# Kernel optimization log

Measured on AMD Instinct MI355X. Metric: run time of the kernel, lower is better.

## Reference

```python
import jax, jax.numpy as jnp
import numpy as np

B, N, D, R = 2, 256, 128, 32

def _sh_l1(r):
    # e3nn-style component-normalized l=1 spherical harmonics of unit vectors
    return jnp.sqrt(3.0) * r

def _sh_l2(r):
    x, y, z = r[..., 0], r[..., 1], r[..., 2]
    c = jnp.sqrt(15.0)
    return jnp.stack([
        c * x * y,
        c * y * z,
        0.5 * jnp.sqrt(5.0) * (3.0 * z * z - 1.0),  # x^2+y^2+z^2 = 1
        c * x * z,
        0.5 * c * (x * x - y * y),
    ], axis=-1)

def _radial(rbf, w1, b1, w2, b2):
    h = rbf @ w1 + b1
    return (h * jax.nn.sigmoid(h)) @ w2 + b2  # Linear -> SiLU -> Linear

def _layernorm(x, g, b, eps=1e-5):
    m = jnp.mean(x, axis=-1, keepdims=True)
    v = jnp.var(x, axis=-1, keepdims=True)
    return (x - m) * jax.lax.rsqrt(v + eps) * g + b

def setup_inputs() -> dict:
    key = jax.random.key(0)
    ks = iter(jax.random.split(key, 40))
    def nrm(shape, s=1.0):
        return jax.random.normal(next(ks), shape, dtype=jnp.float32) * s
    r_hat = nrm((B, N, N, 3))
    r_hat = r_hat / (jnp.linalg.norm(r_hat, axis=-1, keepdims=True) + 1e-9)
    inp = {
        'node_s': nrm((B, N, D)),
        'node_v': nrm((B, N, 3, D)),
        'node_t': nrm((B, N, 5, D)),
        'rbf': jax.random.uniform(next(ks), (B, N, N, R), dtype=jnp.float32),
        'r_hat': r_hat,
        'mask': jnp.ones((B, N, N), dtype=jnp.float32),
    }
    s1, s2 = 1.0 / np.sqrt(R), 1.0 / np.sqrt(D)
    for p in ('r0', 'r1', 'r2', 'r110'):
        inp[p + '_w1'] = nrm((R, D), s1)
        inp[p + '_b1'] = jnp.zeros((D,), jnp.float32)
        inp[p + '_w2'] = nrm((D, D), s2)
        inp[p + '_b2'] = jnp.zeros((D,), jnp.float32)
    inp['src_w'] = nrm((D, D), s2)
    inp['ln_g'] = jnp.ones((D,), jnp.float32)
    inp['ln_b'] = jnp.zeros((D,), jnp.float32)
    inp['out_w'] = nrm((D, D), s2)
    inp['out_b'] = jnp.zeros((D,), jnp.float32)
    inp['v_scale'] = jnp.ones((D,), jnp.float32)
    inp['t_scale'] = jnp.ones((D,), jnp.float32)
    return inp

def reference(node_s, node_v, node_t, rbf, r_hat, mask,
              r0_w1, r0_b1, r0_w2, r0_b2,
              r1_w1, r1_b1, r1_w2, r1_b2,
              r2_w1, r2_b1, r2_w2, r2_b2,
              r110_w1, r110_b1, r110_w2, r110_b2,
              src_w, ln_g, ln_b, out_w, out_b, v_scale, t_scale):
    h = node_s @ src_w                               # (B,N,D)
    h_j = h[:, None, :, :] * mask[..., None]         # (B,N,N,D): h_j[b,i,j]=h[b,j]*mask[b,i,j]
    Y1 = _sh_l1(r_hat)                               # (B,N,N,3)
    Y2 = _sh_l2(r_hat)                               # (B,N,N,5)

    msg_s = jnp.sum(h_j * _radial(rbf, r0_w1, r0_b1, r0_w2, r0_b2), axis=2)  # (B,N,D)
    delta_v = jnp.einsum('bijd,bijc->bicd',
                         h_j * _radial(rbf, r1_w1, r1_b1, r1_w2, r1_b2), Y1) * v_scale
    delta_t = jnp.einsum('bijd,bijc->bicd',
                         h_j * _radial(rbf, r2_w1, r2_b1, r2_w2, r2_b2), Y2) * t_scale

    # v_j[b,i,j] = node_v[b,i] (per the torch unsqueeze(2).expand)
    dot_vY1 = jnp.einsum('bicd,bijc->bijd', node_v, Y1)                      # (B,N,N,D)
    msg_s_from_v = jnp.sum(dot_vY1 * _radial(rbf, r110_w1, r110_b1, r110_w2, r110_b2)
                           * mask[..., None], axis=2)                        # (B,N,D)

    delta_s = _layernorm(msg_s + msg_s_from_v, ln_g, ln_b) @ out_w + out_b
    return (delta_s, delta_v, delta_t)
```

## Files before the change

### kernel.cpp

```cpp
#include <hip/hip_runtime.h>

#define Bb 2
#define Nn 256
#define Dd 128
#define Rr 32

typedef unsigned short u16;
typedef unsigned int   u32;
typedef __attribute__((ext_vector_type(8))) short bf16x8;
typedef __attribute__((ext_vector_type(4))) float f32x4;
typedef __attribute__((ext_vector_type(2))) u32   u32x2;
typedef __attribute__((ext_vector_type(4))) u32   u32x4;

__device__ u16 g_w1t[4*Dd*Rr];
__device__ u16 g_w2t[4*Dd*Dd];

__device__ __forceinline__ short f2bfs(float f){
  u32 u = __float_as_uint(f);
  u += 0x7FFFu + ((u >> 16) & 1u);
  return (short)(u >> 16);
}
__device__ __forceinline__ u16 f2bf(float f){
  u32 u = __float_as_uint(f);
  u += 0x7FFFu + ((u >> 16) & 1u);
  return (u16)(u >> 16);
}
__device__ __forceinline__ u32 cvtpk(float a, float b){
  u32 r;
  asm("v_cvt_pk_bf16_f32 %0, %1, %2" : "=v"(r) : "v"(a), "v"(b));
  return r;
}
__device__ __forceinline__ int swz(int j){
  return (j&3) | ((((j>>2)^(j>>3))&1)<<2);
}

__global__ __launch_bounds__(128) void prep_kernel(
    const float* __restrict__ node_s, const float* __restrict__ src_w,
    const float* __restrict__ r0w1, const float* __restrict__ r1w1,
    const float* __restrict__ r2w1, const float* __restrict__ r3w1,
    const float* __restrict__ r0w2, const float* __restrict__ r1w2,
    const float* __restrict__ r2w2, const float* __restrict__ r3w2,
    float* __restrict__ h_out)
{
  const int bx = blockIdx.x;
  const int t  = threadIdx.x;
  if (bx < Bb*Nn){
    __shared__ float s_row[Dd];
    s_row[t] = node_s[(size_t)bx*Dd + t];
    __syncthreads();
    float acc = 0.f;
    #pragma unroll 8
    for (int k=0;k<Dd;k++) acc += s_row[k]*src_w[k*Dd + t];
    const int b = bx >> 8, i = bx & 255;
    h_out[(size_t)(b*Dd + t)*Nn + i] = acc;
  } else {
    const int kb = bx - Bb*Nn;
    const int p  = kb >> 3, sl = kb & 7;
    const float* W1 = (p==0)?r0w1:(p==1)?r1w1:(p==2)?r2w1:r3w1;
    const float* W2 = (p==0)?r0w2:(p==1)?r1w2:(p==2)?r2w2:r3w2;
    u16* W1T = g_w1t + p*Dd*Rr;
    u16* W2T = g_w2t + p*Dd*Dd;
    #pragma unroll
    for (int it=0; it<4; it++){
      int in = sl*512 + it*128 + t;
      W1T[(in & 127)*Rr + (in >> 7)] = f2bf(W1[in]);
    }
    #pragma unroll
    for (int it=0; it<16; it++){
      int in = sl*2048 + it*128 + t;
      W2T[(in & 127)*Dd + (in >> 7)] = f2bf(W2[in]);
    }
  }
}

__global__ __launch_bounds__(512,4) void se3_mfma13(
    const float* __restrict__ node_v,
    const float* __restrict__ rbf,
    const float* __restrict__ r_hat,
    const float* __restrict__ maskp,
    const float* __restrict__ r0b1, const float* __restrict__ r0b2,
    const float* __restrict__ r1b1, const float* __restrict__ r1b2,
    const float* __restrict__ r2b1, const float* __restrict__ r2b2,
    const float* __restrict__ r3b1, const float* __restrict__ r3b2,
    const float* __restrict__ ln_g, const float* __restrict__ ln_b,
    const float* __restrict__ out_w, const float* __restrict__ out_b,
    const float* __restrict__ v_scale, const float* __restrict__ t_scale,
    const float* __restrict__ h_ws,
    float* __restrict__ out_s, float* __restrict__ out_v, float* __restrict__ out_t)
{
  __shared__ u16   s_rbf[Nn*40];
  __shared__ u16   s_hid[2*64*128];
  __shared__ u16   s_YT[10*264];
  __shared__ u16   s_Y1r[3*264];
  __shared__ float s_msg[Dd];
  __shared__ float s_xn[Dd];
  __shared__ float s_part[4*Dd];
  __shared__ float s_mv[2];

  const int tid  = threadIdx.x;
  const int bi   = blockIdx.x;
  const int b    = bi >> 8;
  const int lane = tid & 63;
  const int w    = tid >> 6;
  const int q    = lane >> 4;
  const int cc   = lane & 15;
  const int dwb  = w*16;

  if (tid < Nn){
    int j = tid;
    size_t pidx = (size_t)bi*Nn + j;
    float mk = maskp[pidx];
    float x = r_hat[pidx*3+0];
    float y = r_hat[pidx*3+1];
    float z = r_hat[pidx*3+2];
    const float SQ3=1.7320508075688772f;
    const float C15=3.8729833462074170f;
    const float C5H=1.1180339887498949f;
    float y1a=SQ3*x, y1b=SQ3*y, y1c=SQ3*z;
    s_YT[0*264+j]=f2bf(mk);
    s_YT[1*264+j]=f2bf(y1a*mk);
    s_YT[2*264+j]=f2bf(y1b*mk);
    s_YT[3*264+j]=f2bf(y1c*mk);
    s_YT[4*264+j]=f2bf(C15*x*y*mk);
    s_YT[5*264+j]=f2bf(C15*y*z*mk);
    s_YT[6*264+j]=f2bf(C5H*(3.f*z*z-1.f)*mk);
    s_YT[7*264+j]=f2bf(C15*x*z*mk);
    s_YT[8*264+j]=f2bf(0.5f*C15*(x*x-y*y)*mk);
    s_YT[9*264+j]=f2bf(mk);
    s_Y1r[0*264+j]=f2bf(y1a);
    s_Y1r[1*264+j]=f2bf(y1b);
    s_Y1r[2*264+j]=f2bf(y1c);
  }

  const float* rbf_blk = rbf + (size_t)bi*Nn*Rr;
  const float* htb     = h_ws + (size_t)b*Dd*Nn;

  for (int idx=tid; idx<Nn*Rr/2; idx+=512){
    int j = idx >> 4, r2 = (idx & 15)*2;
    const float* src = &rbf_blk[j*Rr + r2];
    float v0 = src[0], v1 = src[1];
    *(u32*)&s_rbf[j*40 + r2] = cvtpk(v0, v1);
  }

  bf16x8 vBf;
  {
    const float* nv = node_v + (size_t)bi*3*Dd;
    int dd = dwb+cc;
    bf16x8 t = {0,0,0,0,0,0,0,0};
    if (q==0){
      t[0]=f2bfs(nv[0*Dd+dd]);
      t[1]=f2bfs(nv[1*Dd+dd]);
      t[2]=f2bfs(nv[2*Dd+dd]);
    }
    vBf=t;
  }

  __syncthreads();

  const f32x4 zf = {0.f,0.f,0.f,0.f};
  f32x4 accred = zf;
  const u16* ytrow = &s_YT[(cc<10?cc:9)*264];

  auto do_gemm1 = [&](int chn, int bufn, const bf16x8& w1f_, const f32x4& b1v_){
    #pragma unroll 1
    for (int jt=0;jt<4;jt++){
      const int jrow = jt*16 + cc;
      bf16x8 rbff = *(const bf16x8*)&s_rbf[(chn*64 + jrow)*40 + q*8];
      f32x4 hc = __builtin_amdgcn_mfma_f32_16x16x32_bf16(w1f_, rbff, zf, 0,0,0);
      float s[4];
      #pragma unroll
      for (int r=0;r<4;r++){
        float x  = hc[r] + b1v_[r];
        float e  = __expf(-x);
        s[r]     = x*__builtin_amdgcn_rcpf(1.f+e);
      }
      u32x2 pk = { cvtpk(s[0], s[1]), cvtpk(s[2], s[3]) };
      const int c0 = w*2 + (q>>1);
      *(u32x2*)&s_hid[bufn*8192 + jrow*128 + ((c0 ^ swz(jrow))<<3) + (q&1)*4] = pk;
    }
  };

  int buf = 0;
  bf16x8 w1f;  f32x4 b1v4;
  bf16x8 w2f[4]; float b2v; u32 gmask;

  w1f  = *(const bf16x8*)&g_w1t[(dwb+cc)*Rr + q*8];
  b1v4 = *(const f32x4*)&r0b1[dwb + q*4];
  do_gemm1(0, 0, w1f, b1v4);

  #pragma unroll 1
  for (int t=0;t<16;t++){
    const int p = t>>2, ch = t&3;
    if (ch==0){
      const u16* W2T = g_w2t + p*Dd*Dd;
      #pragma unroll
      for (int ks=0;ks<4;ks++)
        w2f[ks] = *(const bf16x8*)&W2T[(dwb+cc)*Dd + ks*32 + q*8];
      const float* B2p = (p==0)?r0b2:(p==1)?r1b2:(p==2)?r2b2:r3b2;
      b2v = B2p[dwb + cc];
      const int lo = (p==0)?0:(p==1)?1:(p==2)?4:9;
      const int hi = (p==0)?0:(p==1)?3:(p==2)?8:9;
      gmask = (cc>=lo && cc<=hi) ? 0xFFFFFFFFu : 0u;
    }
    __syncthreads();

    if (t<15){
      const int tn=t+1, pn=tn>>2, chn=tn&3;
      if (chn==0){
        w1f  = *(const bf16x8*)&g_w1t[pn*Dd*Rr + (dwb+cc)*Rr + q*8];
        const float* B1p = (pn==1)?r1b1:(pn==2)?r2b1:r3b1;
        b1v4 = *(const f32x4*)&B1p[dwb + q*4];
      }
      do_gemm1(chn, buf^1, w1f, b1v4);
    }

    #pragma unroll 1
    for (int g=0; g<2; g++){
      u32 bB[4];
      #pragma unroll 1
      for (int mm=0;mm<2;mm++){
        const int jp = g*32 + ((cc>>2)<<3) + mm*4 + (cc&3);
        bf16x8 af[4];
        #pragma unroll
        for (int ks=0;ks<4;ks++)
          af[ks] = *(const bf16x8*)&s_hid[buf*8192 + jp*128 + (((ks*4+q) ^ swz(jp))<<3)];

        f32x4 dotC;
        if (p==3){
          bf16x8 aY = {0,0,0,0,0,0,0,0};
          if (q==0){
            int jg = ch*64 + jp;
            aY[0]=(short)s_Y1r[0*264+jg];
            aY[1]=(short)s_Y1r[1*264+jg];
            aY[2]=(short)s_Y1r[2*264+jg];
          }
          dotC = __builtin_amdgcn_mfma_f32_16x16x32_bf16(aY, vBf, zf, 0,0,0);
        }

        f32x4 c2 = zf;
        #pragma unroll
        for (int ks=0;ks<4;ks++)
          c2 = __builtin_amdgcn_mfma_f32_16x16x32_bf16(af[ks], w2f[ks], c2, 0,0,0);
        float gg[4];
        if (p<3){
          f32x4 hq = *(const f32x4*)&htb[(size_t)(dwb+cc)*Nn + ch*64 + g*32 + q*8 + mm*4];
          #pragma unroll
          for (int r=0;r<4;r++)
            gg[r] = (c2[r]+b2v) * hq[r];
        } else {
          #pragma unroll
          for (int r=0;r<4;r++)
            gg[r] = (c2[r]+b2v) * dotC[r];
        }
        bB[mm*2+0] = cvtpk(gg[0], gg[1]);
        bB[mm*2+1] = cvtpk(gg[2], gg[3]);
      }
      bf16x8 aR = *(const bf16x8*)(ytrow + ch*64 + g*32 + q*8);
      u32* arp = (u32*)&aR;
      arp[0]&=gmask; arp[1]&=gmask; arp[2]&=gmask; arp[3]&=gmask;
      u32x4 bw = { bB[0], bB[1], bB[2], bB[3] };
      bf16x8 bG = __builtin_bit_cast(bf16x8, bw);
      accred = __builtin_amdgcn_mfma_f32_16x16x32_bf16(aR, bG, accred, 0,0,0);
    }
    buf ^= 1;
  }

  {
    const int d = dwb + cc;
    #pragma unroll
    for (int r=0;r<4;r++){
      const int rw = q*4 + r;
      float val = accred[r];
      if (rw==0)      s_msg[d] = val;
      else if (rw<=3) out_v[(size_t)bi*3*Dd + (size_t)(rw-1)*Dd + d] = val*v_scale[d];
      else if (rw<=8) out_t[(size_t)bi*5*Dd + (size_t)(rw-4)*Dd + d] = val*t_scale[d];
      else if (rw==9) s_xn[d] = val;
    }
  }
  __syncthreads();

  if (tid < 64){
    float a0=s_msg[tid]+s_xn[tid], a1=s_msg[tid+64]+s_xn[tid+64];
    float s1=a0+a1, s2=a0*a0+a1*a1;
    #pragma unroll
    for (int off=1;off<64;off<<=1){
      s1 += __shfl_xor(s1,off);
      s2 += __shfl_xor(s2,off);
    }
    if (tid==0){
      float m   = s1*(1.f/Dd);
      float var = fmaxf(s2*(1.f/Dd) - m*m, 0.f);
      s_mv[0]=m;
      s_mv[1]=rsqrtf(var+1e-5f);
    }
  }
  __syncthreads();
  if (tid < Dd){
    float msg = s_msg[tid]+s_xn[tid];
    s_xn[tid] = (msg - s_mv[0])*s_mv[1]*ln_g[tid] + ln_b[tid];
  }
  __syncthreads();

  {
    int dp = tid & 127, seg = tid >> 7;
    float pa = 0.f;
    #pragma unroll 8
    for (int k=seg*32;k<seg*32+32;k++)
      pa += s_xn[k]*out_w[k*Dd+dp];
    s_part[seg*Dd+dp]=pa;
  }
  __syncthreads();
  if (tid < Dd)
    out_s[(size_t)bi*Dd+tid] = s_part[tid]+s_part[Dd+tid]+s_part[2*Dd+tid]+s_part[3*Dd+tid]+out_b[tid];
}

extern "C" void kernel_launch(void* const* d_in, const int* in_sizes, int n_in,
                              void* d_out, int out_size, void* d_ws, size_t ws_size,
                              hipStream_t stream) {
  const float* node_s = (const float*)d_in[0];
  const float* node_v = (const float*)d_in[1];
  const float* rbf    = (const float*)d_in[3];
  const float* r_hat  = (const float*)d_in[4];
  const float* maskp  = (const float*)d_in[5];
  const float* r0w1=(const float*)d_in[6],  *r0b1=(const float*)d_in[7];
  const float* r0w2=(const float*)d_in[8],  *r0b2=(const float*)d_in[9];
  const float* r1w1=(const float*)d_in[10], *r1b1=(const float*)d_in[11];
  const float* r1w2=(const float*)d_in[12], *r1b2=(const float*)d_in[13];
  const float* r2w1=(const float*)d_in[14], *r2b1=(const float*)d_in[15];
  const float* r2w2=(const float*)d_in[16], *r2b2=(const float*)d_in[17];
  const float* r3w1=(const float*)d_in[18], *r3b1=(const float*)d_in[19];
  const float* r3w2=(const float*)d_in[20], *r3b2=(const float*)d_in[21];
  const float* src_w  =(const float*)d_in[22];
  const float* ln_g   =(const float*)d_in[23];
  const float* ln_b   =(const float*)d_in[24];
  const float* out_w  =(const float*)d_in[25];
  const float* out_b  =(const float*)d_in[26];
  const float* v_scale=(const float*)d_in[27];
  const float* t_scale=(const float*)d_in[28];

  float* h_ws = (float*)d_ws;
  float* out_s = (float*)d_out;
  float* out_v = out_s + (size_t)Bb*Nn*Dd;
  float* out_t = out_v + (size_t)Bb*Nn*3*Dd;

  prep_kernel<<<dim3(Bb*Nn + 32), dim3(128), 0, stream>>>(
      node_s, src_w,
      r0w1, r1w1, r2w1, r3w1, r0w2, r1w2, r2w2, r3w2,
      h_ws);
  se3_mfma13<<<dim3(Bb*Nn), dim3(512), 0, stream>>>(
      node_v, rbf, r_hat, maskp,
      r0b1,r0b2, r1b1,r1b2, r2b1,r2b2, r3b1,r3b2,
      ln_g, ln_b, out_w, out_b, v_scale, t_scale,
      h_ws, out_s, out_v, out_t);
}
```

Before: 184.5 us.

## Unroll chunk pipeline per radial net and pad hidden buffer instead of swizzle

Restructures the 16-step loop into an outer loop over the four radial nets with the four chunks manually unrolled, so each gemm1/gemm2 stage has constant buffer and chunk indices and the inner loops can be fully unrolled. The XOR swizzle on the shared hidden buffer is replaced by a padded row stride of 130, and the gather mask AND is replaced by pointing inactive lanes at an added zero row of Y. Per-chunk h loads are hoisted ahead of the MFMAs. The aim is less index arithmetic and more instruction-level overlap, at the cost of more registers and code size, which may hurt occupancy under the 512x4 launch bound.

```diff
diff --git a/kernel.cpp b/kernel.cpp
--- a/kernel.cpp
+++ b/kernel.cpp
@@ -29,9 +29,6 @@
   u32 r;
   asm("v_cvt_pk_bf16_f32 %0, %1, %2" : "=v"(r) : "v"(a), "v"(b));
   return r;
-}
-__device__ __forceinline__ int swz(int j){
-  return (j&3) | ((((j>>2)^(j>>3))&1)<<2);
 }
 
 __global__ __launch_bounds__(128) void prep_kernel(
@@ -73,7 +70,7 @@
   }
 }
 
-__global__ __launch_bounds__(512,4) void se3_mfma13(
+__global__ __launch_bounds__(512,4) void se3_mfma14(
     const float* __restrict__ node_v,
     const float* __restrict__ rbf,
     const float* __restrict__ r_hat,
@@ -89,8 +86,8 @@
     float* __restrict__ out_s, float* __restrict__ out_v, float* __restrict__ out_t)
 {
   __shared__ u16   s_rbf[Nn*40];
-  __shared__ u16   s_hid[2*64*128];
-  __shared__ u16   s_YT[10*264];
+  __shared__ u16   s_hid[2*64*130];
+  __shared__ u16   s_YT[11*264];
   __shared__ u16   s_Y1r[3*264];
   __shared__ float s_msg[Dd];
   __shared__ float s_xn[Dd];
@@ -104,6 +101,7 @@
   const int w    = tid >> 6;
   const int q    = lane >> 4;
   const int cc   = lane & 15;
+  const int hi5  = cc >> 2, lo2 = cc & 3;
   const int dwb  = w*16;
 
   if (tid < Nn){
@@ -127,6 +125,7 @@
     s_YT[7*264+j]=f2bf(C15*x*z*mk);
     s_YT[8*264+j]=f2bf(0.5f*C15*(x*x-y*y)*mk);
     s_YT[9*264+j]=f2bf(mk);
+    s_YT[10*264+j]=0;
     s_Y1r[0*264+j]=f2bf(y1a);
     s_Y1r[1*264+j]=f2bf(y1b);
     s_Y1r[2*264+j]=f2bf(y1c);
@@ -155,43 +154,97 @@
     vBf=t;
   }
 
+  const int rbf_base = cc*40 + q*8;
+  const int hw_base  = cc*130 + w*16 + q*4;
+  const int af_base  = (hi5*8+lo2)*130 + q*8;
+
   __syncthreads();
 
   const f32x4 zf = {0.f,0.f,0.f,0.f};
   f32x4 accred = zf;
-  const u16* ytrow = &s_YT[(cc<10?cc:9)*264];
-
-  auto do_gemm1 = [&](int chn, int bufn, const bf16x8& w1f_, const f32x4& b1v_){
-    #pragma unroll 1
+
+  bf16x8 w1f;  f32x4 b1v4;
+  bf16x8 w2f[4]; float b2v;
+  const u16* ytq;
+
+  auto do_gemm1 = [&](int chn, int bufn){
+    #pragma unroll
     for (int jt=0;jt<4;jt++){
-      const int jrow = jt*16 + cc;
-      bf16x8 rbff = *(const bf16x8*)&s_rbf[(chn*64 + jrow)*40 + q*8];
-      f32x4 hc = __builtin_amdgcn_mfma_f32_16x16x32_bf16(w1f_, rbff, zf, 0,0,0);
-      float s[4];
+      bf16x8 rbff = *(const bf16x8*)&s_rbf[rbf_base + chn*2560 + jt*640];
+      f32x4 hc = __builtin_amdgcn_mfma_f32_16x16x32_bf16(w1f, rbff, zf, 0,0,0);
+      float s0,s1,s2,s3;
+      {
+        float x0=hc[0]+b1v4[0], x1=hc[1]+b1v4[1], x2=hc[2]+b1v4[2], x3=hc[3]+b1v4[3];
+        s0 = x0*__builtin_amdgcn_rcpf(1.f+__expf(-x0));
+        s1 = x1*__builtin_amdgcn_rcpf(1.f+__expf(-x1));
+        s2 = x2*__builtin_amdgcn_rcpf(1.f+__expf(-x2));
+        s3 = x3*__builtin_amdgcn_rcpf(1.f+__expf(-x3));
+      }
+      u32x2 pk = { cvtpk(s0, s1), cvtpk(s2, s3) };
+      *(u32x2*)&s_hid[bufn*8320 + hw_base + jt*2080] = pk;
+    }
+  };
+
+  auto do_gemm2 = [&](int chx, int bufx, int p){
+    f32x4 hql[2][2];
+    if (p<3){
       #pragma unroll
-      for (int r=0;r<4;r++){
-        float x  = hc[r] + b1v_[r];
-        float e  = __expf(-x);
-        s[r]     = x*__builtin_amdgcn_rcpf(1.f+e);
+      for (int g=0;g<2;g++)
+        #pragma unroll
+        for (int mm=0;mm<2;mm++)
+          hql[g][mm] = *(const f32x4*)&htb[(size_t)(dwb+cc)*Nn + chx*64 + g*32 + q*8 + mm*4];
+    }
+    #pragma unroll
+    for (int g=0; g<2; g++){
+      u32 bB[4];
+      #pragma unroll
+      for (int mm=0;mm<2;mm++){
+        bf16x8 af[4];
+        #pragma unroll
+        for (int ks=0;ks<4;ks++)
+          af[ks] = *(const bf16x8*)&s_hid[bufx*8320 + af_base + g*4160 + mm*520 + ks*32];
+
+        f32x4 dotC;
+        if (p==3){
+          bf16x8 aY = {0,0,0,0,0,0,0,0};
+          if (q==0){
+            int jg = chx*64 + g*32 + hi5*8 + mm*4 + lo2;
+            aY[0]=(short)s_Y1r[0*264+jg];
+            aY[1]=(short)s_Y1r[1*264+jg];
+            aY[2]=(short)s_Y1r[2*264+jg];
+          }
+          dotC = __builtin_amdgcn_mfma_f32_16x16x32_bf16(aY, vBf, zf, 0,0,0);
+        }
+
+        f32x4 c2 = zf;
+        #pragma unroll
+        for (int ks=0;ks<4;ks++)
+          c2 = __builtin_amdgcn_mfma_f32_16x16x32_bf16(af[ks], w2f[ks], c2, 0,0,0);
+        float g0,g1,g2,g3;
+        if (p<3){
+          g0=(c2[0]+b2v)*hql[g][mm][0]; g1=(c2[1]+b2v)*hql[g][mm][1];
+          g2=(c2[2]+b2v)*hql[g][mm][2]; g3=(c2[3]+b2v)*hql[g][mm][3];
+        } else {
+          g0=(c2[0]+b2v)*dotC[0]; g1=(c2[1]+b2v)*dotC[1];
+          g2=(c2[2]+b2v)*dotC[2]; g3=(c2[3]+b2v)*dotC[3];
+        }
+        bB[mm*2+0] = cvtpk(g0, g1);
+        bB[mm*2+1] = cvtpk(g2, g3);
       }
-      u32x2 pk = { cvtpk(s[0], s[1]), cvtpk(s[2], s[3]) };
-      const int c0 = w*2 + (q>>1);
-      *(u32x2*)&s_hid[bufn*8192 + jrow*128 + ((c0 ^ swz(jrow))<<3) + (q&1)*4] = pk;
+      bf16x8 aR = *(const bf16x8*)(ytq + chx*64 + g*32);
+      u32x4 bw = { bB[0], bB[1], bB[2], bB[3] };
+      bf16x8 bG = __builtin_bit_cast(bf16x8, bw);
+      accred = __builtin_amdgcn_mfma_f32_16x16x32_bf16(aR, bG, accred, 0,0,0);
     }
   };
-
-  int buf = 0;
-  bf16x8 w1f;  f32x4 b1v4;
-  bf16x8 w2f[4]; float b2v; u32 gmask;
 
   w1f  = *(const bf16x8*)&g_w1t[(dwb+cc)*Rr + q*8];
   b1v4 = *(const f32x4*)&r0b1[dwb + q*4];
-  do_gemm1(0, 0, w1f, b1v4);
+  do_gemm1(0, 0);
 
   #pragma unroll 1
-  for (int t=0;t<16;t++){
-    const int p = t>>2, ch = t&3;
-    if (ch==0){
+  for (int p=0;p<4;p++){
+    {
       const u16* W2T = g_w2t + p*Dd*Dd;
       #pragma unroll
       for (int ks=0;ks<4;ks++)
@@ -200,69 +253,19 @@
       b2v = B2p[dwb + cc];
       const int lo = (p==0)?0:(p==1)?1:(p==2)?4:9;
       const int hi = (p==0)?0:(p==1)?3:(p==2)?8:9;
-      gmask = (cc>=lo && cc<=hi) ? 0xFFFFFFFFu : 0u;
-    }
+      ytq = &s_YT[((cc>=lo && cc<=hi)?cc:10)*264] + q*8;
+    }
+    __syncthreads(); do_gemm1(1,1); do_gemm2(0,0,p);
+    __syncthreads(); do_gemm1(2,0); do_gemm2(1,1,p);
+    __syncthreads(); do_gemm1(3,1); do_gemm2(2,0,p);
     __syncthreads();
-
-    if (t<15){
-      const int tn=t+1, pn=tn>>2, chn=tn&3;
-      if (chn==0){
-        w1f  = *(const bf16x8*)&g_w1t[pn*Dd*Rr + (dwb+cc)*Rr + q*8];
-        const float* B1p = (pn==1)?r1b1:(pn==2)?r2b1:r3b1;
-        b1v4 = *(const f32x4*)&B1p[dwb + q*4];
-      }
-      do_gemm1(chn, buf^1, w1f, b1v4);
-    }
-
-    #pragma unroll 1
-    for (int g=0; g<2; g++){
-      u32 bB[4];
-      #pragma unroll 1
-      for (int mm=0;mm<2;mm++){
-        const int jp = g*32 + ((cc>>2)<<3) + mm*4 + (cc&3);
-        bf16x8 af[4];
-        #pragma unroll
-        for (int ks=0;ks<4;ks++)
-          af[ks] = *(const bf16x8*)&s_hid[buf*8192 + jp*128 + (((ks*4+q) ^ swz(jp))<<3)];
-
-        f32x4 dotC;
-        if (p==3){
-          bf16x8 aY = {0,0,0,0,0,0,0,0};
-          if (q==0){
-            int jg = ch*64 + jp;
-            aY[0]=(short)s_Y1r[0*264+jg];
-            aY[1]=(short)s_Y1r[1*264+jg];
-            aY[2]=(short)s_Y1r[2*264+jg];
-          }
-          dotC = __builtin_amdgcn_mfma_f32_16x16x32_bf16(aY, vBf, zf, 0,0,0);
-        }
-
-        f32x4 c2 = zf;
-        #pragma unroll
-        for (int ks=0;ks<4;ks++)
-          c2 = __builtin_amdgcn_mfma_f32_16x16x32_bf16(af[ks], w2f[ks], c2, 0,0,0);
-        float gg[4];
-        if (p<3){
-          f32x4 hq = *(const f32x4*)&htb[(size_t)(dwb+cc)*Nn + ch*64 + g*32 + q*8 + mm*4];
-          #pragma unroll
-          for (int r=0;r<4;r++)
-            gg[r] = (c2[r]+b2v) * hq[r];
-        } else {
-          #pragma unroll
-          for (int r=0;r<4;r++)
-            gg[r] = (c2[r]+b2v) * dotC[r];
-        }
-        bB[mm*2+0] = cvtpk(gg[0], gg[1]);
-        bB[mm*2+1] = cvtpk(gg[2], gg[3]);
-      }
-      bf16x8 aR = *(const bf16x8*)(ytrow + ch*64 + g*32 + q*8);
-      u32* arp = (u32*)&aR;
-      arp[0]&=gmask; arp[1]&=gmask; arp[2]&=gmask; arp[3]&=gmask;
-      u32x4 bw = { bB[0], bB[1], bB[2], bB[3] };
-      bf16x8 bG = __builtin_bit_cast(bf16x8, bw);
-      accred = __builtin_amdgcn_mfma_f32_16x16x32_bf16(aR, bG, accred, 0,0,0);
-    }
-    buf ^= 1;
+    if (p<3){
+      w1f  = *(const bf16x8*)&g_w1t[(p+1)*Dd*Rr + (dwb+cc)*Rr + q*8];
+      const float* B1n = (p==0)?r1b1:(p==1)?r2b1:r3b1;
+      b1v4 = *(const f32x4*)&B1n[dwb + q*4];
+      do_gemm1(0,0);
+    }
+    do_gemm2(3,1,p);
   }
 
   {
@@ -347,7 +350,7 @@
       node_s, src_w,
       r0w1, r1w1, r2w1, r3w1, r0w2, r1w2, r2w2, r3w2,
       h_ws);
-  se3_mfma13<<<dim3(Bb*Nn), dim3(512), 0, stream>>>(
+  se3_mfma14<<<dim3(Bb*Nn), dim3(512), 0, stream>>>(
       node_v, rbf, r_hat, maskp,
       r0b1,r0b2, r1b1,r1b2, r2b1,r2b2, r3b1,r3b2,
       ln_g, ln_b, out_w, out_b, v_scale, t_scale,
```

Measured after the change: 185.7 us. Within noise of the previous version (+0.7%).
